# Kernel tuning notes

Measured on AMD Instinct MI355X. Metric: run time of the kernel, lower is better.

The kernel has to match this reference:

```python
import jax, jax.numpy as jnp
import numpy as np

B, L, S, D, H, NS, NSLOT = 2, 2048, 2048, 1024, 16, 8, 512
HD = D // H


def _silu(x):
    return x * jax.nn.sigmoid(x)


def _layernorm(x, g, b, eps=1e-5):
    mu = jnp.mean(x, axis=-1, keepdims=True)
    var = jnp.var(x, axis=-1, keepdims=True)
    return (x - mu) * jax.lax.rsqrt(var + eps) * g + b


def setup_inputs() -> dict:
    key = jax.random.key(0)
    ks = jax.random.split(key, 12)
    x_q = jax.random.normal(ks[0], (B, L, D), dtype=jnp.float32)
    x_idx = jax.random.randint(ks[1], (B, S), 0, NSLOT)
    E_slots = jax.random.normal(ks[2], (NSLOT, D), dtype=jnp.float32)
    # EMA decay rates close to 1 so multi-scale gates stay non-degenerate over S steps
    rhos = 1.0 - 0.005 * jax.random.uniform(ks[3], (NS,), dtype=jnp.float32)
    C_seq = jax.random.uniform(ks[4], (B, L, NS), dtype=jnp.float32)
    s = 1.0 / np.sqrt(D)
    Wq = jax.random.normal(ks[5], (D, D), dtype=jnp.float32) * s
    Wk = jax.random.normal(ks[6], (D, D), dtype=jnp.float32) * s
    Wv = jax.random.normal(ks[7], (D, D), dtype=jnp.float32) * s
    Wo = jax.random.normal(ks[8], (D, D), dtype=jnp.float32) * s
    Wpe = jax.random.normal(ks[9], (D, NS), dtype=jnp.float32) * (1.0 / np.sqrt(NS))
    ln_kv_g = jnp.ones((D,), jnp.float32); ln_kv_b = jnp.zeros((D,), jnp.float32)
    ln_q_g = jnp.ones((D,), jnp.float32); ln_q_b = jnp.zeros((D,), jnp.float32)
    return dict(x_q=x_q, x_idx=x_idx, E_slots=E_slots, rhos=rhos, C_seq=C_seq,
                Wq=Wq, Wk=Wk, Wv=Wv, Wo=Wo, Wpe=Wpe,
                ln_kv_g=ln_kv_g, ln_kv_b=ln_kv_b, ln_q_g=ln_q_g, ln_q_b=ln_q_b)


def reference(x_q, x_idx, E_slots, rhos, C_seq, Wq, Wk, Wv, Wo, Wpe,
              ln_kv_g, ln_kv_b, ln_q_g, ln_q_b):
    # --- KV side: memory = ln_kv(E_slots); K/V = proj(memory); gather by slot id ---
    mem = _layernorm(E_slots, ln_kv_g, ln_kv_b)          # [NSLOT, D]
    Ek = mem @ Wk.T                                       # [NSLOT, D]
    Ev = mem @ Wv.T
    K = Ek[x_idx]                                         # [B, S, D] embedding lookup
    V = Ev[x_idx]
    # --- multiplicative EMA gate per kv position: c[s,m] = rho_m^(age) ---
    ages = (S - 1 - jnp.arange(S)).astype(x_q.dtype)      # [S]
    c_kv = jnp.power(rhos[None, :], ages[:, None])        # [S, NS]
    gate_kv = _silu(c_kv @ Wpe.T)                         # [S, D] = SiLU(pe_proj(C))
    K = K * gate_kv[None]
    V = V * gate_kv[None]
    # --- symmetric query gating: Q = q_proj(ln_q(x_q * SiLU(pe_proj(C_seq)))) ---
    gate_q = _silu(C_seq @ Wpe.T)                         # [B, L, D]
    Q = _layernorm(x_q * gate_q, ln_q_g, ln_q_b) @ Wq.T   # [B, L, D]
    # --- multi-head softmax attention ---
    q = Q.reshape(B, L, H, HD)
    k = K.reshape(B, S, H, HD)
    v = V.reshape(B, S, H, HD)
    scores = jnp.einsum('blhd,bshd->bhls', q, k) / np.sqrt(HD).astype(np.float32)
    attn = jax.nn.softmax(scores, axis=-1)                # [B, H, L, S]
    out = jnp.einsum('bhls,bshd->blhd', attn, v).reshape(B, L, D)
    return out @ Wo.T                                     # o_proj (dropout = identity, eval)
```

## Files before the change

### kernel.cpp

```cpp
#include <hip/hip_runtime.h>
#include <cmath>
#include <cstddef>

namespace {

constexpr int cB = 2, cL = 2048, cS = 2048, cD = 1024, cH = 16, cNS = 8, cNSLOT = 512, cHD = 64;

typedef __attribute__((ext_vector_type(8))) short short8;
typedef __attribute__((ext_vector_type(4))) float f32x4;

#define MFMA16(a, b, c) __builtin_amdgcn_mfma_f32_16x16x32_bf16((a), (b), (c), 0, 0, 0)

__device__ __forceinline__ float sigmoidf_(float x) { return 1.f / (1.f + __expf(-x)); }

__device__ __forceinline__ unsigned short f2bf(float x) {
  union { float f; unsigned u; } c; c.f = x;
  unsigned r = c.u + 0x7FFFu + ((c.u >> 16) & 1u);
  return (unsigned short)(r >> 16);
}
__device__ __forceinline__ float bf2f(unsigned short h) {
  union { unsigned u; float f; } c; c.u = ((unsigned)h) << 16;
  return c.f;
}

__device__ __forceinline__ void unpack8(const uint4 a, const uint4 b, short8& p0, short8& p1) {
  const unsigned p[8] = {a.x, a.y, a.z, a.w, b.x, b.y, b.z, b.w};
  union { unsigned u[4]; short8 s; } H, L;
#pragma unroll
  for (int i = 0; i < 4; i++) {
    H.u[i] = __builtin_amdgcn_perm(p[2 * i + 1], p[2 * i], 0x05040100u);
    L.u[i] = __builtin_amdgcn_perm(p[2 * i + 1], p[2 * i], 0x07060302u);
  }
  p0 = H.s;
  p1 = L.s;
}

__device__ __forceinline__ void async16(const void* g, void* l) {
  __builtin_amdgcn_global_load_lds((const __attribute__((address_space(1))) void*)g,
                                   (__attribute__((address_space(3))) void*)l, 16, 0, 0);
}

__global__ __launch_bounds__(256) void prep_all_kernel(
    const float* __restrict__ Wq, const float* __restrict__ Wk,
    const float* __restrict__ Wv, const float* __restrict__ Wo,
    unsigned short* __restrict__ Wqh, unsigned short* __restrict__ Wql,
    unsigned short* __restrict__ Wkh, unsigned short* __restrict__ Wkl,
    unsigned short* __restrict__ Wvh, unsigned short* __restrict__ Wvl,
    unsigned short* __restrict__ Woh, unsigned short* __restrict__ Wol,
    const float* __restrict__ E, const float* __restrict__ lnkv_g,
    const float* __restrict__ lnkv_b, unsigned short* __restrict__ mh,
    const float* __restrict__ rhos,
    const float* __restrict__ Wpe, float* __restrict__ gkv,
    const float* __restrict__ xq, const float* __restrict__ Cseq,
    const float* __restrict__ lnq_g, const float* __restrict__ lnq_b,
    unsigned short* __restrict__ Yh) {
  __shared__ float sC[cNS];
  __shared__ float rbuf[8];
  const int bid = blockIdx.x;
  const int tid = threadIdx.x;

  if (bid < 2048) {
    const int wid = bid >> 9;
    const size_t off = ((size_t)(bid & 511) * 256 + tid) * 8;
    const float* src = wid == 0 ? Wq : wid == 1 ? Wk : wid == 2 ? Wv : Wo;
    unsigned short* dh = wid == 0 ? Wqh : wid == 1 ? Wkh : wid == 2 ? Wvh : Woh;
    unsigned short* dl = wid == 0 ? Wql : wid == 1 ? Wkl : wid == 2 ? Wvl : Wol;
    const float4 a = *(const float4*)(src + off);
    const float4 b = *(const float4*)(src + off + 4);
    float v[8] = {a.x, a.y, a.z, a.w, b.x, b.y, b.z, b.w};
    unsigned short h8[8], l8[8];
#pragma unroll
    for (int j = 0; j < 8; j++) {
      h8[j] = f2bf(v[j]);
      l8[j] = f2bf(v[j] - bf2f(h8[j]));
    }
    *(uint4*)(dh + off) = *(uint4*)h8;
    *(uint4*)(dl + off) = *(uint4*)l8;
  } else if (bid < 2560) {
    const int row = bid - 2048;
    const int d0 = tid * 4;
    const float4 x = *(const float4*)(E + (size_t)row * cD + d0);
    float s1 = x.x + x.y + x.z + x.w;
    float s2 = x.x * x.x + x.y * x.y + x.z * x.z + x.w * x.w;
#pragma unroll
    for (int o = 32; o > 0; o >>= 1) { s1 += __shfl_xor(s1, o, 64); s2 += __shfl_xor(s2, o, 64); }
    if ((tid & 63) == 0) { rbuf[tid >> 6] = s1; rbuf[4 + (tid >> 6)] = s2; }
    __syncthreads();
    s1 = rbuf[0] + rbuf[1] + rbuf[2] + rbuf[3];
    s2 = rbuf[4] + rbuf[5] + rbuf[6] + rbuf[7];
    const float mean = s1 * (1.f / cD);
    const float var = s2 * (1.f / cD) - mean * mean;
    const float inv = rsqrtf(var + 1e-5f);
    const float4 g = *(const float4*)(lnkv_g + d0);
    const float4 b = *(const float4*)(lnkv_b + d0);
    unsigned short h4[4];
    h4[0] = f2bf((x.x - mean) * inv * g.x + b.x);
    h4[1] = f2bf((x.y - mean) * inv * g.y + b.y);
    h4[2] = f2bf((x.z - mean) * inv * g.z + b.z);
    h4[3] = f2bf((x.w - mean) * inv * g.w + b.w);
    *(uint2*)(mh + (size_t)row * cD + d0) = *(uint2*)h4;
  } else if (bid < 4608) {
    const int s = bid - 2560;
    if (tid < cNS) {
      const float age = (float)(cS - 1 - s);
      sC[tid] = __expf(age * __logf(rhos[tid]));
    }
    __syncthreads();
    const int d0 = tid * 4;
    float4 o4;
#pragma unroll
    for (int j = 0; j < 4; j++) {
      const float* wr = Wpe + (size_t)(d0 + j) * cNS;
      float gs = 0.f;
#pragma unroll
      for (int m = 0; m < cNS; m++) gs += sC[m] * wr[m];
      ((float*)&o4)[j] = gs * sigmoidf_(gs);
    }
    *(float4*)(gkv + (size_t)s * cD + d0) = o4;
  } else {
    const int row = bid - 4608;
    if (tid < cNS) sC[tid] = Cseq[(size_t)row * cNS + tid];
    __syncthreads();
    const int d0 = tid * 4;
    const float4 x = *(const float4*)(xq + (size_t)row * cD + d0);
    float y[4];
    float s1 = 0.f, s2 = 0.f;
#pragma unroll
    for (int j = 0; j < 4; j++) {
      const float* wr = Wpe + (size_t)(d0 + j) * cNS;
      float gs = 0.f;
#pragma unroll
      for (int m = 0; m < cNS; m++) gs += sC[m] * wr[m];
      const float val = ((const float*)&x)[j] * gs * sigmoidf_(gs);
      y[j] = val;
      s1 += val;
      s2 += val * val;
    }
#pragma unroll
    for (int o = 32; o > 0; o >>= 1) { s1 += __shfl_xor(s1, o, 64); s2 += __shfl_xor(s2, o, 64); }
    if ((tid & 63) == 0) { rbuf[tid >> 6] = s1; rbuf[4 + (tid >> 6)] = s2; }
    __syncthreads();
    s1 = rbuf[0] + rbuf[1] + rbuf[2] + rbuf[3];
    s2 = rbuf[4] + rbuf[5] + rbuf[6] + rbuf[7];
    const float mean = s1 * (1.f / cD);
    const float var = s2 * (1.f / cD) - mean * mean;
    const float inv = rsqrtf(var + 1e-5f);
    const float4 g = *(const float4*)(lnq_g + d0);
    const float4 b = *(const float4*)(lnq_b + d0);
    unsigned short h4[4];
    h4[0] = f2bf((y[0] - mean) * inv * g.x + b.x);
    h4[1] = f2bf((y[1] - mean) * inv * g.y + b.y);
    h4[2] = f2bf((y[2] - mean) * inv * g.z + b.z);
    h4[3] = f2bf((y[3] - mean) * inv * g.w + b.w);
    *(uint2*)(Yh + (size_t)row * cD + d0) = *(uint2*)h4;
  }
}

template <int MODE>
__device__ __forceinline__ void gemm2_body(
    const unsigned short* __restrict__ Ahi,
    const unsigned short* __restrict__ Whi, const unsigned short* __restrict__ Wlo,
    float* __restrict__ Cf, unsigned short* __restrict__ Chi,
    int m0, int n0, int N, int K, float scale,
    unsigned short* sA, unsigned short* sBh, unsigned short* sBl) {
  const int tid = threadIdx.x;
  const int wave = tid >> 6, lane = tid & 63;
  const int quad = lane >> 4, l16 = lane & 15;
  const int wy = wave >> 1, wx = wave & 1;
  const int sg = (lane & 3) ^ ((lane >> 3) & 3);

  f32x4 acc[4][2];
#pragma unroll
  for (int i = 0; i < 4; i++)
#pragma unroll
    for (int j = 0; j < 2; j++) acc[i][j] = (f32x4){0.f, 0.f, 0.f, 0.f};

  auto stage = [&](int buf, int k0) {
#pragma unroll
    for (int c = 0; c < 2; c++) {
      const int row = c * 64 + wave * 16 + (lane >> 2);
      const size_t ga = (size_t)(m0 + row) * K + k0 + sg * 8;
      async16(Ahi + ga, sA + buf * 4096 + (c * 64 + wave * 16) * 32);
    }
    const int rowb = wave * 16 + (lane >> 2);
    const size_t gb = (size_t)(n0 + rowb) * K + k0 + sg * 8;
    async16(Whi + gb, sBh + buf * 2048 + wave * 16 * 32);
    async16(Wlo + gb, sBl + buf * 2048 + wave * 16 * 32);
  };

  stage(0, 0);
  __syncthreads();
  const int aswz = (l16 >> 1) & 3;
  int buf = 0;
  for (int k0 = 0; k0 < K; k0 += 32, buf ^= 1) {
    if (k0 + 32 < K) stage(buf ^ 1, k0 + 32);
    short8 bh[2], bl2[2];
#pragma unroll
    for (int tj = 0; tj < 2; tj++) {
      const int br = (wx * 32 + tj * 16 + l16) * 32 + ((quad ^ aswz) * 8);
      bh[tj] = *(const short8*)(sBh + buf * 2048 + br);
      bl2[tj] = *(const short8*)(sBl + buf * 2048 + br);
    }
#pragma unroll
    for (int ti = 0; ti < 4; ti++) {
      const int ar = (wy * 64 + ti * 16 + l16) * 32 + ((quad ^ aswz) * 8);
      const short8 ah = *(const short8*)(sA + buf * 4096 + ar);
#pragma unroll
      for (int tj = 0; tj < 2; tj++) {
        acc[ti][tj] = MFMA16(ah, bh[tj], acc[ti][tj]);
        acc[ti][tj] = MFMA16(ah, bl2[tj], acc[ti][tj]);
      }
    }
    __syncthreads();
  }

#pragma unroll
  for (int ti = 0; ti < 4; ti++)
#pragma unroll
    for (int tj = 0; tj < 2; tj++) {
      const int row = m0 + wy * 64 + ti * 16 + quad * 4;
      const int col = n0 + wx * 32 + tj * 16 + l16;
#pragma unroll
      for (int r = 0; r < 4; r++) {
        const size_t idx = (size_t)(row + r) * N + col;
        if constexpr (MODE == 0) {
          Cf[idx] = acc[ti][tj][r];
        } else {
          Chi[idx] = f2bf(acc[ti][tj][r] * scale);
        }
      }
    }
}

__global__ __launch_bounds__(256, 3) void gemm_qkv_kernel(
    const unsigned short* __restrict__ memhi,
    const unsigned short* __restrict__ Wkhi, const unsigned short* __restrict__ Wklo,
    const unsigned short* __restrict__ Wvhi, const unsigned short* __restrict__ Wvlo,
    float* __restrict__ Ek, float* __restrict__ Ev,
    const unsigned short* __restrict__ Yhi,
    const unsigned short* __restrict__ Wqhi, const unsigned short* __restrict__ Wqlo,
    unsigned short* __restrict__ qhi, float qscale) {
  __shared__ __align__(16) unsigned short sA[2 * 128 * 32];
  __shared__ __align__(16) unsigned short sBh[2 * 64 * 32];
  __shared__ __align__(16) unsigned short sBl[2 * 64 * 32];
  const int bid = blockIdx.x;
  if (bid < 128) {
    const int z = bid >> 6, rem = bid & 63;
    const int m0 = (rem >> 4) * 128, n0 = (rem & 15) * 64;
    gemm2_body<0>(memhi, z ? Wvhi : Wkhi, z ? Wvlo : Wklo, z ? Ev : Ek, nullptr,
                  m0, n0, cD, cD, 1.f, sA, sBh, sBl);
  } else {
    const int lid = bid - 128;
    const int m0 = (lid >> 4) * 128, n0 = (lid & 15) * 64;
    gemm2_body<1>(Yhi, Wqhi, Wqlo, nullptr, qhi, m0, n0, cD, cD, qscale, sA, sBh, sBl);
  }
}

__global__ __launch_bounds__(256, 3) void gemm_o_kernel(
    const unsigned short* __restrict__ AOhi,
    const unsigned short* __restrict__ Wohi, const unsigned short* __restrict__ Wolo,
    float* __restrict__ out) {
  __shared__ __align__(16) unsigned short sA[2 * 128 * 32];
  __shared__ __align__(16) unsigned short sBh[2 * 64 * 32];
  __shared__ __align__(16) unsigned short sBl[2 * 64 * 32];
  gemm2_body<0>(AOhi, Wohi, Wolo, out, nullptr, blockIdx.y * 128, blockIdx.x * 64,
                cD, cD, 1.f, sA, sBh, sBl);
}

__global__ __launch_bounds__(256) void prep_kv_kernel(
    const float* __restrict__ Ek, const float* __restrict__ Ev,
    const float* __restrict__ gkv, const int* __restrict__ xidx,
    unsigned short* __restrict__ Khi, unsigned short* __restrict__ Vthi) {
  __shared__ float tile[64][65];
  const int bid = blockIdx.x;
  const int tid = threadIdx.x;
  if (bid < 2048) {
    const int t = bid * 256 + tid;
    const int d0 = (t & 127) * 8;
    const int s = (t >> 7) & (cS - 1);
    const int b = t >> 18;
    const int slot = xidx[b * cS + s];
    const float4 e0 = *(const float4*)(Ek + (size_t)slot * cD + d0);
    const float4 e1 = *(const float4*)(Ek + (size_t)slot * cD + d0 + 4);
    const float4 g0 = *(const float4*)(gkv + (size_t)s * cD + d0);
    const float4 g1 = *(const float4*)(gkv + (size_t)s * cD + d0 + 4);
    float v[8] = {e0.x * g0.x, e0.y * g0.y, e0.z * g0.z, e0.w * g0.w,
                  e1.x * g1.x, e1.y * g1.y, e1.z * g1.z, e1.w * g1.w};
    unsigned short h8[8];
#pragma unroll
    for (int j = 0; j < 8; j++) h8[j] = f2bf(v[j]);
    *(uint4*)(Khi + (size_t)(b * cS + s) * cD + d0) = *(uint4*)h8;
  } else {
    const int local = bid - 2048;
    const int s0 = (local & 31) * 64;
    const int d0 = ((local >> 5) & 15) * 64;
    const int b = local >> 9;
    const int sl = tid >> 4;
    const int dl = (tid & 15) * 4;
#pragma unroll
    for (int it = 0; it < 4; it++) {
      const int s = s0 + sl + it * 16;
      const int slot = xidx[b * cS + s];
      const float4 e = *(const float4*)(Ev + (size_t)slot * cD + d0 + dl);
      const float4 g = *(const float4*)(gkv + (size_t)s * cD + d0 + dl);
      tile[sl + it * 16][dl + 0] = e.x * g.x;
      tile[sl + it * 16][dl + 1] = e.y * g.y;
      tile[sl + it * 16][dl + 2] = e.z * g.z;
      tile[sl + it * 16][dl + 3] = e.w * g.w;
    }
    __syncthreads();
    const int dr = tid >> 3;
    const int sc = (tid & 7) * 8;
#pragma unroll
    for (int it = 0; it < 2; it++) {
      const int d = d0 + dr + it * 32;
      unsigned short h8[8];
#pragma unroll
      for (int j = 0; j < 8; j++) h8[j] = f2bf(tile[sc + j][dr + it * 32]);
      *(uint4*)(Vthi + (size_t)(b * cD + d) * cS + s0 + sc) = *(uint4*)h8;
    }
  }
}

__global__ __launch_bounds__(128, 3) void attn_mfma_kernel(
    const unsigned short* __restrict__ qhi,
    const unsigned short* __restrict__ Khi,
    const unsigned short* __restrict__ Vthi,
    unsigned short* __restrict__ AOhi) {
  __shared__ __align__(16) unsigned short sKh[64 * 64];
  __shared__ __align__(16) unsigned short sVh[64 * 64];
  __shared__ __align__(16) unsigned int sP32[2][16][68];

  const int tid = threadIdx.x;
  const int wave = tid >> 6, lane = tid & 63;
  const int quad = lane >> 4, l16 = lane & 15;
  const int lB = blockIdx.x * 64;
  const int h = blockIdx.y, b = blockIdx.z;

  short8 qh[2][2];
#pragma unroll
  for (int t = 0; t < 2; t++) {
    const size_t base =
        (size_t)(b * cL + lB + wave * 32 + t * 16 + l16) * cD + h * cHD + quad * 8;
    qh[t][0] = *(const short8*)(qhi + base);
    qh[t][1] = *(const short8*)(qhi + base + 32);
  }

  short8 ones;
#pragma unroll
  for (int i = 0; i < 8; i++) ones[i] = (short)0x3F80;

  f32x4 O[2][4], dacc[2];
#pragma unroll
  for (int t = 0; t < 2; t++) {
#pragma unroll
    for (int i = 0; i < 4; i++) O[t][i] = (f32x4){0.f, 0.f, 0.f, 0.f};
    dacc[t] = (f32x4){0.f, 0.f, 0.f, 0.f};
  }

  const int srow8 = lane >> 3;
  const int sg = (lane & 7) ^ srow8;

  const int r0 = (wave * 4 + 0) * 8 + srow8;
  const int r1 = (wave * 4 + 1) * 8 + srow8;
  const int r2 = (wave * 4 + 2) * 8 + srow8;
  const int r3 = (wave * 4 + 3) * 8 + srow8;
  const size_t kb0 = (size_t)(b * cS + r0) * cD + h * cHD + sg * 8;
  const size_t kb1 = (size_t)(b * cS + r1) * cD + h * cHD + sg * 8;
  const size_t kb2 = (size_t)(b * cS + r2) * cD + h * cHD + sg * 8;
  const size_t kb3 = (size_t)(b * cS + r3) * cD + h * cHD + sg * 8;
  const size_t vb0 = (size_t)(b * cD + h * cHD + r0) * cS + sg * 8;
  const size_t vb1 = (size_t)(b * cD + h * cHD + r1) * cS + sg * 8;
  const size_t vb2 = (size_t)(b * cD + h * cHD + r2) * cS + sg * 8;
  const size_t vb3 = (size_t)(b * cD + h * cHD + r3) * cS + sg * 8;

  uint4 k0, k1, k2, k3, v0, v1, v2, v3;
  k0 = *(const uint4*)(Khi + kb0);
  k1 = *(const uint4*)(Khi + kb1);
  k2 = *(const uint4*)(Khi + kb2);
  k3 = *(const uint4*)(Khi + kb3);
  v0 = *(const uint4*)(Vthi + vb0);
  v1 = *(const uint4*)(Vthi + vb1);
  v2 = *(const uint4*)(Vthi + vb2);
  v3 = *(const uint4*)(Vthi + vb3);

  const int j0 = wave * 4;

  for (int s0 = 0; s0 < cS; s0 += 64) {
    __syncthreads();
    *(uint4*)&sKh[(j0 + 0) * 512 + lane * 8] = k0;
    *(uint4*)&sKh[(j0 + 1) * 512 + lane * 8] = k1;
    *(uint4*)&sKh[(j0 + 2) * 512 + lane * 8] = k2;
    *(uint4*)&sKh[(j0 + 3) * 512 + lane * 8] = k3;
    *(uint4*)&sVh[(j0 + 0) * 512 + lane * 8] = v0;
    *(uint4*)&sVh[(j0 + 1) * 512 + lane * 8] = v1;
    *(uint4*)&sVh[(j0 + 2) * 512 + lane * 8] = v2;
    *(uint4*)&sVh[(j0 + 3) * 512 + lane * 8] = v3;
    __syncthreads();

    {
      const int sn = (s0 + 64) & (cS - 1);
      const size_t kc = (size_t)sn * cD;
      k0 = *(const uint4*)(Khi + kb0 + kc);
      k1 = *(const uint4*)(Khi + kb1 + kc);
      k2 = *(const uint4*)(Khi + kb2 + kc);
      k3 = *(const uint4*)(Khi + kb3 + kc);
      v0 = *(const uint4*)(Vthi + vb0 + sn);
      v1 = *(const uint4*)(Vthi + vb1 + sn);
      v2 = *(const uint4*)(Vthi + vb2 + sn);
      v3 = *(const uint4*)(Vthi + vb3 + sn);
    }

    f32x4 sc[2][4];
#pragma unroll
    for (int t = 0; t < 2; t++)
#pragma unroll
      for (int st = 0; st < 4; st++) sc[t][st] = (f32x4){0.f, 0.f, 0.f, 0.f};
    __builtin_amdgcn_s_setprio(1);
#pragma unroll
    for (int st = 0; st < 4; st++) {
      const int srw = st * 16 + l16;
#pragma unroll
      for (int ks = 0; ks < 2; ks++) {
        const int slot = (ks * 4 + quad) ^ (srw & 7);
        const short8 kfh = *(const short8*)&sKh[srw * 64 + slot * 8];
        sc[0][st] = MFMA16(qh[0][ks], kfh, sc[0][st]);
        sc[1][st] = MFMA16(qh[1][ks], kfh, sc[1][st]);
      }
    }
    __builtin_amdgcn_s_setprio(0);

#pragma unroll
    for (int st = 0; st < 4; st++)
#pragma unroll
      for (int r = 0; r < 4; r++) {
        const float e0 = __builtin_amdgcn_exp2f(sc[0][st][r]);
        const float e1 = __builtin_amdgcn_exp2f(sc[1][st][r]);
        unsigned pk;
        asm("v_cvt_pk_bf16_f32 %0, %1, %2" : "=v"(pk) : "v"(e0), "v"(e1));
        sP32[wave][quad * 4 + r][st * 16 + l16] = pk;
      }

    short8 pf0[2], pf1[2];
#pragma unroll
    for (int ss = 0; ss < 2; ss++) {
      const uint4 pa = *(const uint4*)&sP32[wave][l16][ss * 32 + quad * 8];
      const uint4 pb = *(const uint4*)&sP32[wave][l16][ss * 32 + quad * 8 + 4];
      unpack8(pa, pb, pf0[ss], pf1[ss]);
    }

    __builtin_amdgcn_s_setprio(1);
#pragma unroll
    for (int dt = 0; dt < 4; dt++) {
      const int drw = dt * 16 + l16;
#pragma unroll
      for (int ss = 0; ss < 2; ss++) {
        const int slot = (ss * 4 + quad) ^ (drw & 7);
        const short8 vfh = *(const short8*)&sVh[drw * 64 + slot * 8];
        O[0][dt] = MFMA16(pf0[ss], vfh, O[0][dt]);
        O[1][dt] = MFMA16(pf1[ss], vfh, O[1][dt]);
      }
    }
    dacc[0] = MFMA16(pf0[0], ones, dacc[0]);
    dacc[0] = MFMA16(pf0[1], ones, dacc[0]);
    dacc[1] = MFMA16(pf1[0], ones, dacc[1]);
    dacc[1] = MFMA16(pf1[1], ones, dacc[1]);
    __builtin_amdgcn_s_setprio(0);
  }

#pragma unroll
  for (int t = 0; t < 2; t++) {
    float inv[4];
#pragma unroll
    for (int r = 0; r < 4; r++) inv[r] = 1.f / dacc[t][r];
#pragma unroll
    for (int dt = 0; dt < 4; dt++)
#pragma unroll
      for (int r = 0; r < 4; r++) {
        const size_t l = (size_t)(b * cL + lB + wave * 32 + t * 16 + quad * 4 + r);
        AOhi[l * cD + h * cHD + dt * 16 + l16] = f2bf(O[t][dt][r] * inv[r]);
      }
  }
}

}

extern "C" void kernel_launch(void* const* d_in, const int* in_sizes, int n_in,
                              void* d_out, int out_size, void* d_ws, size_t ws_size,
                              hipStream_t stream) {
  (void)in_sizes; (void)n_in; (void)out_size; (void)ws_size;
  const float* x_q = (const float*)d_in[0];
  const int* x_idx = (const int*)d_in[1];
  const float* E_slots = (const float*)d_in[2];
  const float* rhos = (const float*)d_in[3];
  const float* C_seq = (const float*)d_in[4];
  const float* Wq = (const float*)d_in[5];
  const float* Wk = (const float*)d_in[6];
  const float* Wv = (const float*)d_in[7];
  const float* Wo = (const float*)d_in[8];
  const float* Wpe = (const float*)d_in[9];
  const float* ln_kv_g = (const float*)d_in[10];
  const float* ln_kv_b = (const float*)d_in[11];
  const float* ln_q_g = (const float*)d_in[12];
  const float* ln_q_b = (const float*)d_in[13];
  float* out = (float*)d_out;

  float* ws = (float*)d_ws;
  unsigned short* memhi = (unsigned short*)(ws + 0);
  unsigned short* Wkhi = (unsigned short*)(ws + 262144);
  unsigned short* Wklo = (unsigned short*)(ws + 786432);
  unsigned short* Wvhi = (unsigned short*)(ws + 1310720);
  unsigned short* Wvlo = (unsigned short*)(ws + 1835008);
  float* gkv = ws + 2359296;
  unsigned short* Wqhi = (unsigned short*)(ws + 4456448);
  unsigned short* Wqlo = (unsigned short*)(ws + 4980736);
  unsigned short* Wohi = (unsigned short*)(ws + 5505024);
  unsigned short* Wolo = (unsigned short*)(ws + 6029312);
  float* Ek = ws + 6553600;
  float* Ev = ws + 7077888;
  unsigned short* Yhi = (unsigned short*)(ws + 7602176);
  unsigned short* AOhi = (unsigned short*)(ws + 7602176);
  unsigned short* qhi = (unsigned short*)(ws + 9699328);
  unsigned short* Khi = (unsigned short*)(ws + 11796480);
  unsigned short* Vthi = (unsigned short*)(ws + 13893632);

  constexpr float kQScale = 0.125f * 1.44269504088896340736f;

  prep_all_kernel<<<8704, 256, 0, stream>>>(
      Wq, Wk, Wv, Wo, Wqhi, Wqlo, Wkhi, Wklo, Wvhi, Wvlo, Wohi, Wolo,
      E_slots, ln_kv_g, ln_kv_b, memhi, rhos, Wpe, gkv,
      x_q, C_seq, ln_q_g, ln_q_b, Yhi);
  gemm_qkv_kernel<<<640, 256, 0, stream>>>(
      memhi, Wkhi, Wklo, Wvhi, Wvlo, Ek, Ev, Yhi, Wqhi, Wqlo, qhi, kQScale);
  prep_kv_kernel<<<3072, 256, 0, stream>>>(Ek, Ev, gkv, x_idx, Khi, Vthi);
  attn_mfma_kernel<<<dim3(cL / 64, cH, cB), 128, 0, stream>>>(qhi, Khi, Vthi, AOhi);
  gemm_o_kernel<<<dim3(16, 32), 256, 0, stream>>>(AOhi, Wohi, Wolo, out);
}
```

Before: 243.7 us.

## Double-buffer K/V tiles with async global-to-LDS loads and swizzle P buffer

Replaces the register-staged K/V prefetch, which needed two barriers per iteration, with double-buffered LDS tiles filled by async direct-to-LDS loads. This leaves one barrier per iteration and removes the register round-trip. The padded P scratch buffer becomes an unpadded one with a rotation swizzle to avoid bank conflicts. LDS use doubles for K/V, and the occupancy hint drops from 3 to 2 blocks per CU, which may reduce latency hiding.

```diff
diff --git a/kernel.cpp b/kernel.cpp
--- a/kernel.cpp
+++ b/kernel.cpp
@@ -322,14 +322,14 @@
   }
 }
 
-__global__ __launch_bounds__(128, 3) void attn_mfma_kernel(
+__global__ __launch_bounds__(128, 2) void attn_mfma_kernel(
     const unsigned short* __restrict__ qhi,
     const unsigned short* __restrict__ Khi,
     const unsigned short* __restrict__ Vthi,
     unsigned short* __restrict__ AOhi) {
-  __shared__ __align__(16) unsigned short sKh[64 * 64];
-  __shared__ __align__(16) unsigned short sVh[64 * 64];
-  __shared__ __align__(16) unsigned int sP32[2][16][68];
+  __shared__ __align__(16) unsigned short sKh[2][64 * 64];
+  __shared__ __align__(16) unsigned short sVh[2][64 * 64];
+  __shared__ __align__(16) unsigned int sP32[2][16][64];
 
   const int tid = threadIdx.x;
   const int wave = tid >> 6, lane = tid & 63;
@@ -360,56 +360,30 @@
 
   const int srow8 = lane >> 3;
   const int sg = (lane & 7) ^ srow8;
-
-  const int r0 = (wave * 4 + 0) * 8 + srow8;
-  const int r1 = (wave * 4 + 1) * 8 + srow8;
-  const int r2 = (wave * 4 + 2) * 8 + srow8;
-  const int r3 = (wave * 4 + 3) * 8 + srow8;
-  const size_t kb0 = (size_t)(b * cS + r0) * cD + h * cHD + sg * 8;
-  const size_t kb1 = (size_t)(b * cS + r1) * cD + h * cHD + sg * 8;
-  const size_t kb2 = (size_t)(b * cS + r2) * cD + h * cHD + sg * 8;
-  const size_t kb3 = (size_t)(b * cS + r3) * cD + h * cHD + sg * 8;
-  const size_t vb0 = (size_t)(b * cD + h * cHD + r0) * cS + sg * 8;
-  const size_t vb1 = (size_t)(b * cD + h * cHD + r1) * cS + sg * 8;
-  const size_t vb2 = (size_t)(b * cD + h * cHD + r2) * cS + sg * 8;
-  const size_t vb3 = (size_t)(b * cD + h * cHD + r3) * cS + sg * 8;
-
-  uint4 k0, k1, k2, k3, v0, v1, v2, v3;
-  k0 = *(const uint4*)(Khi + kb0);
-  k1 = *(const uint4*)(Khi + kb1);
-  k2 = *(const uint4*)(Khi + kb2);
-  k3 = *(const uint4*)(Khi + kb3);
-  v0 = *(const uint4*)(Vthi + vb0);
-  v1 = *(const uint4*)(Vthi + vb1);
-  v2 = *(const uint4*)(Vthi + vb2);
-  v3 = *(const uint4*)(Vthi + vb3);
-
   const int j0 = wave * 4;
 
+  size_t kb[4], vb[4];
+#pragma unroll
+  for (int i = 0; i < 4; i++) {
+    const int r = (j0 + i) * 8 + srow8;
+    kb[i] = (size_t)(b * cS + r) * cD + h * cHD + sg * 8;
+    vb[i] = (size_t)(b * cD + h * cHD + r) * cS + sg * 8;
+  }
+
+  auto stage = [&](int bf, int sn) {
+    const size_t kc = (size_t)sn * cD;
+#pragma unroll
+    for (int i = 0; i < 4; i++) async16(Khi + kb[i] + kc, &sKh[bf][(j0 + i) * 512]);
+#pragma unroll
+    for (int i = 0; i < 4; i++) async16(Vthi + vb[i] + sn, &sVh[bf][(j0 + i) * 512]);
+  };
+
+  stage(0, 0);
+  __syncthreads();
+
+  int buf = 0;
   for (int s0 = 0; s0 < cS; s0 += 64) {
-    __syncthreads();
-    *(uint4*)&sKh[(j0 + 0) * 512 + lane * 8] = k0;
-    *(uint4*)&sKh[(j0 + 1) * 512 + lane * 8] = k1;
-    *(uint4*)&sKh[(j0 + 2) * 512 + lane * 8] = k2;
-    *(uint4*)&sKh[(j0 + 3) * 512 + lane * 8] = k3;
-    *(uint4*)&sVh[(j0 + 0) * 512 + lane * 8] = v0;
-    *(uint4*)&sVh[(j0 + 1) * 512 + lane * 8] = v1;
-    *(uint4*)&sVh[(j0 + 2) * 512 + lane * 8] = v2;
-    *(uint4*)&sVh[(j0 + 3) * 512 + lane * 8] = v3;
-    __syncthreads();
-
-    {
-      const int sn = (s0 + 64) & (cS - 1);
-      const size_t kc = (size_t)sn * cD;
-      k0 = *(const uint4*)(Khi + kb0 + kc);
-      k1 = *(const uint4*)(Khi + kb1 + kc);
-      k2 = *(const uint4*)(Khi + kb2 + kc);
-      k3 = *(const uint4*)(Khi + kb3 + kc);
-      v0 = *(const uint4*)(Vthi + vb0 + sn);
-      v1 = *(const uint4*)(Vthi + vb1 + sn);
-      v2 = *(const uint4*)(Vthi + vb2 + sn);
-      v3 = *(const uint4*)(Vthi + vb3 + sn);
-    }
+    stage(buf ^ 1, (s0 + 64) & (cS - 1));
 
     f32x4 sc[2][4];
 #pragma unroll
@@ -423,7 +397,7 @@
 #pragma unroll
       for (int ks = 0; ks < 2; ks++) {
         const int slot = (ks * 4 + quad) ^ (srw & 7);
-        const short8 kfh = *(const short8*)&sKh[srw * 64 + slot * 8];
+        const short8 kfh = *(const short8*)&sKh[buf][srw * 64 + slot * 8];
         sc[0][st] = MFMA16(qh[0][ks], kfh, sc[0][st]);
         sc[1][st] = MFMA16(qh[1][ks], kfh, sc[1][st]);
       }
@@ -438,15 +412,20 @@
         const float e1 = __builtin_amdgcn_exp2f(sc[1][st][r]);
         unsigned pk;
         asm("v_cvt_pk_bf16_f32 %0, %1, %2" : "=v"(pk) : "v"(e0), "v"(e1));
-        sP32[wave][quad * 4 + r][st * 16 + l16] = pk;
+        const int prow = quad * 4 + r;
+        const int pcol = (st * 16 + l16 + ((prow & 7) << 2)) & 63;
+        sP32[wave][prow][pcol] = pk;
       }
 
     short8 pf0[2], pf1[2];
-#pragma unroll
-    for (int ss = 0; ss < 2; ss++) {
-      const uint4 pa = *(const uint4*)&sP32[wave][l16][ss * 32 + quad * 8];
-      const uint4 pb = *(const uint4*)&sP32[wave][l16][ss * 32 + quad * 8 + 4];
-      unpack8(pa, pb, pf0[ss], pf1[ss]);
+    {
+      const int rrot = (l16 & 7) << 2;
+#pragma unroll
+      for (int ss = 0; ss < 2; ss++) {
+        const uint4 pa = *(const uint4*)&sP32[wave][l16][(ss * 32 + quad * 8 + rrot) & 63];
+        const uint4 pb = *(const uint4*)&sP32[wave][l16][(ss * 32 + quad * 8 + 4 + rrot) & 63];
+        unpack8(pa, pb, pf0[ss], pf1[ss]);
+      }
     }
 
     __builtin_amdgcn_s_setprio(1);
@@ -456,7 +435,7 @@
 #pragma unroll
       for (int ss = 0; ss < 2; ss++) {
         const int slot = (ss * 4 + quad) ^ (drw & 7);
-        const short8 vfh = *(const short8*)&sVh[drw * 64 + slot * 8];
+        const short8 vfh = *(const short8*)&sVh[buf][drw * 64 + slot * 8];
         O[0][dt] = MFMA16(pf0[ss], vfh, O[0][dt]);
         O[1][dt] = MFMA16(pf1[ss], vfh, O[1][dt]);
       }
@@ -466,6 +445,9 @@
     dacc[1] = MFMA16(pf1[0], ones, dacc[1]);
     dacc[1] = MFMA16(pf1[1], ones, dacc[1]);
     __builtin_amdgcn_s_setprio(0);
+
+    __syncthreads();
+    buf ^= 1;
   }
 
 #pragma unroll
```

After: 244.8 us. Within noise of the previous version (+0.5%).
